# Kernel optimization log

Hardware: AMD Instinct MI355X
Metric: run time of the kernel (lower is better)

The kernel has to match this reference:

```python
import jax, jax.numpy as jnp
import numpy as np

NEG_SLOPE = 0.2

def gat_layer(x, src, dst, W, a_src, a_dst, num_nodes):
    """PyG-style GATConv. W:[F_in,H*C], a_src/a_dst:[H,C]. Returns [N,H,C]."""
    H, C = a_src.shape
    h = (x @ W).reshape(num_nodes, H, C)                      # [N,H,C]
    e_src = jnp.sum(h * a_src, axis=-1)                       # [N,H]
    e_dst = jnp.sum(h * a_dst, axis=-1)                       # [N,H]
    e = jax.nn.leaky_relu(e_src[src] + e_dst[dst], NEG_SLOPE) # [E,H]
    # segment softmax over incoming edges of each destination node
    m = jax.ops.segment_max(e, dst, num_segments=num_nodes)
    w = jnp.exp(e - m[dst])
    z = jax.ops.segment_sum(w, dst, num_segments=num_nodes)
    alpha = w / (z[dst] + 1e-16)                               # [E,H]
    msg = h[src] * alpha[:, :, None]                           # [E,H,C]
    return jax.ops.segment_sum(msg, dst, num_segments=num_nodes)


def setup_inputs() -> dict:
    key = jax.random.key(0)
    ks = jax.random.split(key, 16)
    N, E, F_IN, HID, A, G = 50000, 800000, 128, 128, 32, 64
    x = jax.random.normal(ks[0], (N, F_IN), dtype=jnp.float32)
    edge_index = jax.random.randint(ks[1], (2, E), 0, N, dtype=jnp.int32)
    batch = jnp.sort(jax.random.randint(ks[2], (N,), 0, G, dtype=jnp.int32))
    s = 0.1
    W1 = jax.random.normal(ks[3], (F_IN, 2 * HID), jnp.float32) * s
    a_src1 = jax.random.normal(ks[4], (2, HID), jnp.float32) * s
    a_dst1 = jax.random.normal(ks[5], (2, HID), jnp.float32) * s
    b1 = jnp.zeros((2 * HID,), jnp.float32)
    W2 = jax.random.normal(ks[6], (2 * HID, HID), jnp.float32) * s
    a_src2 = jax.random.normal(ks[7], (1, HID), jnp.float32) * s
    a_dst2 = jax.random.normal(ks[8], (1, HID), jnp.float32) * s
    b2 = jnp.zeros((HID,), jnp.float32)
    Wp = jax.random.normal(ks[9], (HID, A), jnp.float32) * s
    bp = jnp.zeros((A,), jnp.float32)
    Wv = jax.random.normal(ks[10], (HID, 1), jnp.float32) * s
    bv = jnp.zeros((1,), jnp.float32)
    return {"x": x, "edge_index": edge_index, "batch": batch,
            "W1": W1, "a_src1": a_src1, "a_dst1": a_dst1, "b1": b1,
            "W2": W2, "a_src2": a_src2, "a_dst2": a_dst2, "b2": b2,
            "Wp": Wp, "bp": bp, "Wv": Wv, "bv": bv}


def reference(x, edge_index, batch, W1, a_src1, a_dst1, b1,
              W2, a_src2, a_dst2, b2, Wp, bp, Wv, bv):
    N = x.shape[0]
    G = 64  # number of graphs in the batch
    # add self-loops (PyG GATConv default)
    loop = jnp.arange(N, dtype=edge_index.dtype)
    src = jnp.concatenate([edge_index[0], loop])
    dst = jnp.concatenate([edge_index[1], loop])
    # layer 1: heads=2, concat=True
    h1 = gat_layer(x, src, dst, W1, a_src1, a_dst1, N)        # [N,2,HID]
    h1 = jax.nn.elu(h1.reshape(N, -1) + b1)                   # [N,2*HID]
    # layer 2: heads=1, concat=False (mean over heads = identity for H=1)
    h2 = gat_layer(h1, src, dst, W2, a_src2, a_dst2, N)       # [N,1,HID]
    h2 = jax.nn.elu(h2.reshape(N, -1) + b2)                   # [N,HID]
    # global mean pool over graphs
    sums = jax.ops.segment_sum(h2, batch, num_segments=G)
    cnt = jax.ops.segment_sum(jnp.ones((N,), h2.dtype), batch, num_segments=G)
    x_pool = sums / jnp.maximum(cnt, 1.0)[:, None]            # [G,HID]
    policy_logits = x_pool @ Wp + bp                          # [G,A]
    state_value = x_pool @ Wv + bv                            # [G,1]
    return (policy_logits, state_value)
```

## Files before the change

kernel.cpp:

```cpp
#include <hip/hip_runtime.h>
#include <hip/hip_bf16.h>
#include <cstdint>


typedef __attribute__((ext_vector_type(8))) short bf16x8;
typedef __attribute__((ext_vector_type(4))) float f32x4;

#define NBLK_H 160
#define BSH 6
#define BMSK 63

__device__ __forceinline__ float wave_sum(float v) {
#pragma unroll
    for (int off = 32; off >= 1; off >>= 1) v += __shfl_xor(v, off, 64);
    return v;
}

__device__ __forceinline__ unsigned short f2bf(float f) {
    union { float f; uint32_t u; } c; c.f = f;
    uint32_t u = c.u;
    return (unsigned short)((u + 0x7fffu + ((u >> 16) & 1u)) >> 16);
}

__device__ __forceinline__ float bf2f(unsigned short u) {
    union { uint32_t u; float f; } c; c.u = ((uint32_t)u) << 16;
    return c.f;
}


template <int K, int FOUT>
__device__ __forceinline__ void swizzle_body(const float* __restrict__ W, int ldW, int colOff,
                                             unsigned short* __restrict__ Bsw, int tid) {
    constexpr int CPW = FOUT / 4, NCT = CPW / 16, KST = K / 32;
    if (tid >= K * FOUT / 8) return;
    int lane = tid & 63;
    int rest = tid >> 6;
    int t = rest % KST; rest /= KST;
    int c = rest % NCT; rest /= NCT;
    int cg_ = rest;
    int quad = lane >> 4, lo = lane & 15;
    int col = colOff + cg_ * CPW + c * 16 + lo;
    unsigned short v[8];
#pragma unroll
    for (int j = 0; j < 8; ++j)
        v[j] = f2bf(W[(t * 32 + quad * 8 + j) * ldW + col]);
    ushort4* dst = (ushort4*)(Bsw + (size_t)tid * 8);
    ushort4 o0, o1;
    o0.x = v[0]; o0.y = v[1]; o0.z = v[2]; o0.w = v[3];
    o1.x = v[4]; o1.y = v[5]; o1.z = v[6]; o1.w = v[7];
    dst[0] = o0; dst[1] = o1;
}


__global__ __launch_bounds__(256) void init_kernel(
        const float* __restrict__ W1, const float* __restrict__ W2,
        const float* __restrict__ a_src1, const float* __restrict__ a_dst1,
        unsigned short* __restrict__ B1h0, unsigned short* __restrict__ B1h1,
        unsigned short* __restrict__ B2,
        float* __restrict__ v1s, float* __restrict__ v1d,
        int* __restrict__ zbase, int zn4, int ZB,
        const int* __restrict__ ei, int* __restrict__ hist,
        int E, int ET, int CHUNK, int NB) {
    __shared__ int bins[1024];
    int b = blockIdx.x;
    if (b < 8)        swizzle_body<128, 128>(W1, 256, 0,   B1h0, b * 256 + threadIdx.x);
    else if (b < 16)  swizzle_body<128, 128>(W1, 256, 128, B1h1, (b - 8) * 256 + threadIdx.x);
    else if (b < 32)  swizzle_body<256, 128>(W2, 128, 0,   B2, (b - 16) * 256 + threadIdx.x);
    else if (b == 32) {
        int t = threadIdx.x, h = t >> 7, k = t & 127;
        float vs = 0.f, vd = 0.f;
        for (int c = 0; c < 128; ++c) {
            float w = W1[k * 256 + h * 128 + c];
            vs += w * a_src1[h * 128 + c];
            vd += w * a_dst1[h * 128 + c];
        }
        v1s[h * 128 + k] = vs;
        v1d[h * 128 + k] = vd;
    } else if (b < 33 + ZB) {
        int i = (b - 33) * 256 + threadIdx.x;
        if (i < zn4) ((int4*)zbase)[i] = make_int4(0, 0, 0, 0);
    } else {
        const int blk = b - 33 - ZB;
        for (int t = threadIdx.x; t < NB; t += 256) bins[t] = 0;
        __syncthreads();
        const int start = blk * CHUNK, end = min(ET, start + CHUNK);
        for (int i = start + threadIdx.x; i < end; i += 256) {
            int dst = (i < E) ? ei[E + i] : (i - E);
            atomicAdd(&bins[dst >> BSH], 1);
        }
        __syncthreads();
        for (int t = threadIdx.x; t < NB; t += 256) hist[t * NBLK_H + blk] = bins[t];
    }
}


__global__ __launch_bounds__(256) void scan_attn1(
        int* __restrict__ hist, int* __restrict__ tsum, int M, int TILESH,
        const float* __restrict__ x, const float* __restrict__ v1s,
        const float* __restrict__ v1d, float* __restrict__ es1,
        float* __restrict__ ed1, unsigned short* __restrict__ xbf, int N) {
    __shared__ int buf[256];
    if ((int)blockIdx.x < TILESH) {
        const int t = threadIdx.x;
        const int base = blockIdx.x * 1024 + t * 4;
        int v[4]; int s = 0;
#pragma unroll
        for (int k = 0; k < 4; ++k) { v[k] = (base + k < M) ? hist[base + k] : 0; s += v[k]; }
        buf[t] = s;
        __syncthreads();
#pragma unroll
        for (int off = 1; off < 256; off <<= 1) {
            int xx = (t >= off) ? buf[t - off] : 0;
            __syncthreads();
            buf[t] += xx;
            __syncthreads();
        }
        int run = buf[t] - s;
#pragma unroll
        for (int k = 0; k < 4; ++k) {
            if (base + k < M) hist[base + k] = run;
            run += v[k];
        }
        if (t == 255) tsum[blockIdx.x] = buf[255];
        return;
    }
    int bid = blockIdx.x - TILESH;
    int wid = (bid * 256 + threadIdx.x) >> 6;
    int lane = threadIdx.x & 63;
    if (wid >= N) return;
    float2 xv = *(const float2*)(x + (size_t)wid * 128 + lane * 2);
    float p0s = xv.x * v1s[lane * 2] + xv.y * v1s[lane * 2 + 1];
    float p1s = xv.x * v1s[128 + lane * 2] + xv.y * v1s[128 + lane * 2 + 1];
    float p0d = xv.x * v1d[lane * 2] + xv.y * v1d[lane * 2 + 1];
    float p1d = xv.x * v1d[128 + lane * 2] + xv.y * v1d[128 + lane * 2 + 1];
    p0s = wave_sum(p0s); p1s = wave_sum(p1s);
    p0d = wave_sum(p0d); p1d = wave_sum(p1d);
    if (lane == 0) {
        es1[wid * 2] = p0s; es1[wid * 2 + 1] = p1s;
        ed1[wid * 2] = p0d; ed1[wid * 2 + 1] = p1d;
    }
    ushort2 o; o.x = f2bf(xv.x); o.y = f2bf(xv.y);
    *(ushort2*)(xbf + (size_t)wid * 128 + lane * 2) = o;
}


__global__ __launch_bounds__(256) void part_kernel(const int* __restrict__ ei,
                                                   const int* __restrict__ hist,
                                                   const int* __restrict__ tsum,
                                                   int* __restrict__ bsorted,
                                                   int* __restrict__ segbase,
                                                   int E, int ET, int CHUNK, int NB, int T) {
    __shared__ int sb[256];
    __shared__ int scur[1024];
    const int t = threadIdx.x;
    sb[t] = (t < T) ? tsum[t] : 0;
    __syncthreads();
#pragma unroll
    for (int off = 1; off < 256; off <<= 1) {
        int v = (t >= off) ? sb[t - off] : 0;
        __syncthreads();
        sb[t] += v;
        __syncthreads();
    }
    const int blk = blockIdx.x;
    for (int b = t; b < NB; b += 256) {
        int idx = b * NBLK_H + blk;
        int tile = idx >> 10;
        int v = hist[idx] + (tile ? sb[tile - 1] : 0);
        scur[b] = v;
        if (blk == 0) segbase[b] = v;
    }
    if (blk == 0 && t == 0) segbase[NB] = sb[T - 1];
    __syncthreads();
    const int start = blk * CHUNK, end = min(ET, start + CHUNK);
    for (int i = start + t; i < end; i += 256) {
        int dst = (i < E) ? ei[E + i] : (i - E);
        int src = (i < E) ? ei[i] : dst;
        int pos = atomicAdd(&scur[dst >> BSH], 1);
        bsorted[pos] = (src << BSH) | (dst & BMSK);
    }
}


__global__ __launch_bounds__(256) void bucket_kernel(const int* __restrict__ bsorted,
                                                     const int* __restrict__ segbase,
                                                     const float* __restrict__ es1,
                                                     const float* __restrict__ ed1,
                                                     int* __restrict__ csr_src,
                                                     float2* __restrict__ csr_alpha,
                                                     int* __restrict__ rowptr,
                                                     int N, int NB) {
    __shared__ int cnt[64], excl[64];
    __shared__ float z0[64], z1[64];
    __shared__ float2 edv[64];
    __shared__ int ebuf[3072];
    __shared__ float2 wbuf[3072];
    const int b = blockIdx.x;
    const int gbase = segbase[b], gend = segbase[b + 1];
    const int sz = gend - gbase;
    const int t = threadIdx.x;
    if (b == 0 && t == 0) rowptr[N] = segbase[NB];
    if (t < 64) {
        cnt[t] = 0; z0[t] = 0.f; z1[t] = 0.f;
        int dst = (b << BSH) + t;
        if (dst < N) edv[t] = *(const float2*)(ed1 + dst * 2);
        else edv[t] = make_float2(0.f, 0.f);
    }
    __syncthreads();
    const bool fits = (sz <= 3072);
    for (int i = t; i < sz; i += 256) {
        int p = bsorted[gbase + i];
        int s = p >> BSH, ld = p & BMSK;
        float2 esv = *(const float2*)(es1 + s * 2);
        float e0 = esv.x + edv[ld].x; e0 = (e0 > 0.f) ? e0 : 0.2f * e0;
        float e1 = esv.y + edv[ld].y; e1 = (e1 > 0.f) ? e1 : 0.2f * e1;
        float w0 = __expf(e0), w1 = __expf(e1);
        if (fits) { ebuf[i] = p; wbuf[i] = make_float2(w0, w1); }
        atomicAdd(&z0[ld], w0);
        atomicAdd(&z1[ld], w1);
        atomicAdd(&cnt[ld], 1);
    }
    __syncthreads();
    if (t < 64) excl[t] = cnt[t];
    __syncthreads();
    for (int off = 1; off < 64; off <<= 1) {
        int v = (t < 64 && t >= off) ? excl[t - off] : 0;
        __syncthreads();
        if (t < 64) excl[t] += v;
        __syncthreads();
    }
    if (t < 64) {
        int dst = (b << BSH) + t;
        if (dst < N) rowptr[dst] = gbase + excl[t] - cnt[t];
    }
    __syncthreads();
    if (t < 64) {
        cnt[t] = excl[t] - cnt[t];
        z0[t] = 1.f / (z0[t] + 1e-16f);
        z1[t] = 1.f / (z1[t] + 1e-16f);
    }
    __syncthreads();
    if (fits) {
        for (int i = t; i < sz; i += 256) {
            int p = ebuf[i]; float2 wv = wbuf[i];
            int ld = p & BMSK;
            int pos = atomicAdd(&cnt[ld], 1);
            csr_src[gbase + pos] = p >> BSH;
            csr_alpha[gbase + pos] = make_float2(wv.x * z0[ld], wv.y * z1[ld]);
        }
    } else {
        for (int i = t; i < sz; i += 256) {
            int p = bsorted[gbase + i];
            int s = p >> BSH, ld = p & BMSK;
            float2 esv = *(const float2*)(es1 + s * 2);
            float e0 = esv.x + edv[ld].x; e0 = (e0 > 0.f) ? e0 : 0.2f * e0;
            float e1 = esv.y + edv[ld].y; e1 = (e1 > 0.f) ? e1 : 0.2f * e1;
            float w0 = __expf(e0), w1 = __expf(e1);
            int pos = atomicAdd(&cnt[ld], 1);
            csr_src[gbase + pos] = s;
            csr_alpha[gbase + pos] = make_float2(w0 * z0[ld], w1 * z1[ld]);
        }
    }
}


#define ACC2(U_, WW_, P_, Q_) { float v_;                              \
    v_ = bf2f(U_.x); P_.x += WW_.x * v_; Q_.x += WW_.y * v_;           \
    v_ = bf2f(U_.y); P_.y += WW_.x * v_; Q_.y += WW_.y * v_;           \
    v_ = bf2f(U_.z); P_.z += WW_.x * v_; Q_.z += WW_.y * v_;           \
    v_ = bf2f(U_.w); P_.w += WW_.x * v_; Q_.w += WW_.y * v_; }

__global__ void gat_agg_x(const unsigned short* __restrict__ xbf,
                          const int* __restrict__ rowptr, const int* __restrict__ csr_src,
                          const float2* __restrict__ csr_alpha,
                          unsigned short* __restrict__ aggx, int N, int NPAD) {
    __shared__ int    s_lds[4][2][32];
    __shared__ float2 a_lds[4][2][32];
    const int wave = threadIdx.x >> 6, lane = threadIdx.x & 63;
    const int g = lane >> 5, c = lane & 31;
    const int node = (blockIdx.x * 4 + wave) * 2 + g;
    if (node >= N) return;
    const int rs = rowptr[node], re = rowptr[node + 1];
    float4 p = {0.f, 0.f, 0.f, 0.f}, q = {0.f, 0.f, 0.f, 0.f};
    for (int i = rs; i < re; i += 32) {
        const int cnt = min(re - i, 32);
        if (c < cnt) {
            s_lds[wave][g][c] = csr_src[i + c];
            a_lds[wave][g][c] = csr_alpha[i + c];
        }
        int k = 0;
        for (; k + 7 < cnt; k += 8) {
            int s0 = s_lds[wave][g][k + 0], s1 = s_lds[wave][g][k + 1];
            int s2 = s_lds[wave][g][k + 2], s3 = s_lds[wave][g][k + 3];
            int s4 = s_lds[wave][g][k + 4], s5 = s_lds[wave][g][k + 5];
            int s6 = s_lds[wave][g][k + 6], s7 = s_lds[wave][g][k + 7];
            float2 a0 = a_lds[wave][g][k + 0], a1 = a_lds[wave][g][k + 1];
            float2 a2 = a_lds[wave][g][k + 2], a3 = a_lds[wave][g][k + 3];
            float2 a4 = a_lds[wave][g][k + 4], a5 = a_lds[wave][g][k + 5];
            float2 a6 = a_lds[wave][g][k + 6], a7 = a_lds[wave][g][k + 7];
            ushort4 u0 = *(const ushort4*)(xbf + (size_t)s0 * 128 + c * 4);
            ushort4 u1 = *(const ushort4*)(xbf + (size_t)s1 * 128 + c * 4);
            ushort4 u2 = *(const ushort4*)(xbf + (size_t)s2 * 128 + c * 4);
            ushort4 u3 = *(const ushort4*)(xbf + (size_t)s3 * 128 + c * 4);
            ushort4 u4 = *(const ushort4*)(xbf + (size_t)s4 * 128 + c * 4);
            ushort4 u5 = *(const ushort4*)(xbf + (size_t)s5 * 128 + c * 4);
            ushort4 u6 = *(const ushort4*)(xbf + (size_t)s6 * 128 + c * 4);
            ushort4 u7 = *(const ushort4*)(xbf + (size_t)s7 * 128 + c * 4);
            ACC2(u0, a0, p, q);
            ACC2(u1, a1, p, q);
            ACC2(u2, a2, p, q);
            ACC2(u3, a3, p, q);
            ACC2(u4, a4, p, q);
            ACC2(u5, a5, p, q);
            ACC2(u6, a6, p, q);
            ACC2(u7, a7, p, q);
        }
        for (; k < cnt; ++k) {
            int s0 = s_lds[wave][g][k];
            float2 a0 = a_lds[wave][g][k];
            ushort4 u0 = *(const ushort4*)(xbf + (size_t)s0 * 128 + c * 4);
            ACC2(u0, a0, p, q);
        }
    }
    ushort4 o;
    o.x = f2bf(p.x); o.y = f2bf(p.y); o.z = f2bf(p.z); o.w = f2bf(p.w);
    *(ushort4*)(aggx + (size_t)node * 128 + c * 4) = o;
    o.x = f2bf(q.x); o.y = f2bf(q.y); o.z = f2bf(q.z); o.w = f2bf(q.w);
    *(ushort4*)(aggx + (size_t)NPAD * 128 + (size_t)node * 128 + c * 4) = o;
}


__global__ __launch_bounds__(256) void gemm12_fused(
        const unsigned short* __restrict__ Abase,
        const unsigned short* __restrict__ B1h0, const unsigned short* __restrict__ B1h1,
        const unsigned short* __restrict__ B2sw,
        const float* __restrict__ b1,
        const float* __restrict__ a_src, const float* __restrict__ a_dst,
        float* __restrict__ es, float* __restrict__ ed,
        unsigned short* __restrict__ C, int N, int NPAD) {
    __shared__ unsigned short h1t[64][264];
    __shared__ float lds_ps[4][64];
    __shared__ float lds_pd[4][64];
    const int tid = threadIdx.x;
    const int wave = tid >> 6, lane = tid & 63;
    const int quad = lane >> 4, lo = lane & 15;
    const int n0 = blockIdx.x * 64;

    {
        const int head = wave >> 1, wh = wave & 1;
        const unsigned short* A = Abase + (size_t)head * NPAD * 128;
        const bf16x8* Bp = (const bf16x8*)(head ? B1h1 : B1h0);
        bf16x8 bf[4][4];
#pragma unroll
        for (int c = 0; c < 4; ++c)
#pragma unroll
            for (int t = 0; t < 4; ++t)
                bf[c][t] = Bp[((wh * 4 + c) * 4 + t) * 64 + lane];
        f32x4 acc[4][4];
#pragma unroll
        for (int r = 0; r < 4; ++r)
#pragma unroll
            for (int c = 0; c < 4; ++c) acc[r][c] = (f32x4){0.f, 0.f, 0.f, 0.f};
#pragma unroll
        for (int r = 0; r < 4; ++r) {
            const unsigned short* Ar = A + (size_t)(n0 + r * 16 + lo) * 128 + quad * 8;
#pragma unroll
            for (int t = 0; t < 4; ++t) {
                bf16x8 af = *(const bf16x8*)(Ar + t * 32);
#pragma unroll
                for (int c = 0; c < 4; ++c)
                    acc[r][c] = __builtin_amdgcn_mfma_f32_16x16x32_bf16(af, bf[c][t],
                                                                       acc[r][c], 0, 0, 0);
            }
        }
#pragma unroll
        for (int r = 0; r < 4; ++r) {
            int rl = r * 16 + quad * 4;
#pragma unroll
            for (int c = 0; c < 4; ++c) {
                int col = head * 128 + wh * 64 + c * 16 + lo;
                float bv = b1[col];
#pragma unroll
                for (int j = 0; j < 4; ++j) {
                    float v = acc[r][c][j] + bv;
                    v = (v > 0.f) ? v : __expf(v) - 1.f;
                    h1t[rl + j][col] = f2bf(v);
                }
            }
        }
    }
    __syncthreads();

    bf16x8 bf2[2][8];
    {
        const bf16x8* Bp2 = (const bf16x8*)B2sw;
#pragma unroll
        for (int c = 0; c < 2; ++c)
#pragma unroll
            for (int t = 0; t < 8; ++t)
                bf2[c][t] = Bp2[((wave * 2 + c) * 8 + t) * 64 + lane];
    }
    f32x4 acc2[4][2];
#pragma unroll
    for (int r = 0; r < 4; ++r)
#pragma unroll
        for (int c = 0; c < 2; ++c) acc2[r][c] = (f32x4){0.f, 0.f, 0.f, 0.f};
#pragma unroll
    for (int r = 0; r < 4; ++r) {
        const unsigned short* Ar = &h1t[r * 16 + lo][quad * 8];
#pragma unroll
        for (int t = 0; t < 8; ++t) {
            bf16x8 af = *(const bf16x8*)(Ar + t * 32);
#pragma unroll
            for (int c = 0; c < 2; ++c)
                acc2[r][c] = __builtin_amdgcn_mfma_f32_16x16x32_bf16(af, bf2[c][t],
                                                                    acc2[r][c], 0, 0, 0);
        }
    }
    const int c0 = wave * 32;
#pragma unroll
    for (int r = 0; r < 4; ++r) {
        int row = n0 + r * 16 + quad * 4;
#pragma unroll
        for (int c = 0; c < 2; ++c) {
            int col = c0 + c * 16 + lo;
#pragma unroll
            for (int j = 0; j < 4; ++j)
                if (row + j < N) C[(size_t)(row + j) * 128 + col] = f2bf(acc2[r][c][j]);
        }
    }
    float asv[2], adv[2];
#pragma unroll
    for (int c = 0; c < 2; ++c) {
        int col = c0 + c * 16 + lo;
        asv[c] = a_src[col];
        adv[c] = a_dst[col];
    }
#pragma unroll
    for (int r = 0; r < 4; ++r) {
#pragma unroll
        for (int j = 0; j < 4; ++j) {
            float ps = 0.f, pd = 0.f;
#pragma unroll
            for (int c = 0; c < 2; ++c) { ps += acc2[r][c][j] * asv[c]; pd += acc2[r][c][j] * adv[c]; }
#pragma unroll
            for (int off = 1; off <= 8; off <<= 1) {
                ps += __shfl_xor(ps, off, 64);
                pd += __shfl_xor(pd, off, 64);
            }
            if (lo == 0) {
                int row_l = r * 16 + quad * 4 + j;
                lds_ps[wave][row_l] = ps;
                lds_pd[wave][row_l] = pd;
            }
        }
    }
    __syncthreads();
    if (tid < 64) {
        int row = tid;
        int n = n0 + row;
        if (n < N) {
            es[n] = lds_ps[0][row] + lds_ps[1][row] + lds_ps[2][row] + lds_ps[3][row];
            ed[n] = lds_pd[0][row] + lds_pd[1][row] + lds_pd[2][row] + lds_pd[3][row];
        }
    }
}


__global__ void alpha2_kernel(const int* __restrict__ rowptr, const int* __restrict__ csr_src,
                              const float* __restrict__ es, const float* __restrict__ ed,
                              float* __restrict__ csr_a2, int N) {
    int wid = (blockIdx.x * blockDim.x + threadIdx.x) >> 6;
    int lane = threadIdx.x & 63;
    if (wid >= N) return;
    const int rs = rowptr[wid], re = rowptr[wid + 1];
    const float edn = ed[wid];
    float z = 0.f;
    for (int i = rs; i < re; i += 64) {
        int cnt = min(re - i, 64);
        if (lane < cnt) {
            int s = csr_src[i + lane];
            float e = es[s] + edn;
            e = (e > 0.f) ? e : 0.2f * e;
            float w = __expf(e);
            csr_a2[i + lane] = w;
            z += w;
        }
    }
    z = wave_sum(z);
    const float rz = 1.f / (z + 1e-16f);
    for (int i = rs + lane; i < re; i += 64) csr_a2[i] *= rz;
}


#define ACC1(U_, W_, P_) {                                   \
    P_.x += W_ * bf2f(U_.x); P_.y += W_ * bf2f(U_.y);        \
    P_.z += W_ * bf2f(U_.z); P_.w += W_ * bf2f(U_.w); }

__global__ void gat_agg_h1(const unsigned short* __restrict__ Hpre,
                           const int* __restrict__ rowptr, const int* __restrict__ csr_src,
                           const float* __restrict__ csr_a2,
                           const float* __restrict__ bias, unsigned short* __restrict__ out,
                           int N) {
    __shared__ int   s_lds[4][2][32];
    __shared__ float a_lds[4][2][32];
    const int wave = threadIdx.x >> 6, lane = threadIdx.x & 63;
    const int g = lane >> 5, c = lane & 31;
    const int node = (blockIdx.x * 4 + wave) * 2 + g;
    if (node >= N) return;
    const int rs = rowptr[node], re = rowptr[node + 1];
    float4 p = {0.f, 0.f, 0.f, 0.f};
    for (int i = rs; i < re; i += 32) {
        const int cnt = min(re - i, 32);
        if (c < cnt) {
            s_lds[wave][g][c] = csr_src[i + c];
            a_lds[wave][g][c] = csr_a2[i + c];
        }
        int k = 0;
        for (; k + 7 < cnt; k += 8) {
            int s0 = s_lds[wave][g][k + 0], s1 = s_lds[wave][g][k + 1];
            int s2 = s_lds[wave][g][k + 2], s3 = s_lds[wave][g][k + 3];
            int s4 = s_lds[wave][g][k + 4], s5 = s_lds[wave][g][k + 5];
            int s6 = s_lds[wave][g][k + 6], s7 = s_lds[wave][g][k + 7];
            float a0 = a_lds[wave][g][k + 0], a1 = a_lds[wave][g][k + 1];
            float a2 = a_lds[wave][g][k + 2], a3 = a_lds[wave][g][k + 3];
            float a4 = a_lds[wave][g][k + 4], a5 = a_lds[wave][g][k + 5];
            float a6 = a_lds[wave][g][k + 6], a7 = a_lds[wave][g][k + 7];
            ushort4 u0 = *(const ushort4*)(Hpre + (size_t)s0 * 128 + c * 4);
            ushort4 u1 = *(const ushort4*)(Hpre + (size_t)s1 * 128 + c * 4);
            ushort4 u2 = *(const ushort4*)(Hpre + (size_t)s2 * 128 + c * 4);
            ushort4 u3 = *(const ushort4*)(Hpre + (size_t)s3 * 128 + c * 4);
            ushort4 u4 = *(const ushort4*)(Hpre + (size_t)s4 * 128 + c * 4);
            ushort4 u5 = *(const ushort4*)(Hpre + (size_t)s5 * 128 + c * 4);
            ushort4 u6 = *(const ushort4*)(Hpre + (size_t)s6 * 128 + c * 4);
            ushort4 u7 = *(const ushort4*)(Hpre + (size_t)s7 * 128 + c * 4);
            ACC1(u0, a0, p);
            ACC1(u1, a1, p);
            ACC1(u2, a2, p);
            ACC1(u3, a3, p);
            ACC1(u4, a4, p);
            ACC1(u5, a5, p);
            ACC1(u6, a6, p);
            ACC1(u7, a7, p);
        }
        for (; k < cnt; ++k) {
            int s0 = s_lds[wave][g][k];
            float a0 = a_lds[wave][g][k];
            ushort4 u0 = *(const ushort4*)(Hpre + (size_t)s0 * 128 + c * 4);
            ACC1(u0, a0, p);
        }
    }
    float4 bv = ((const float4*)bias)[c];
    float ox = p.x + bv.x, oy = p.y + bv.y, oz = p.z + bv.z, ow = p.w + bv.w;
    ox = (ox > 0.f) ? ox : __expf(ox) - 1.f;
    oy = (oy > 0.f) ? oy : __expf(oy) - 1.f;
    oz = (oz > 0.f) ? oz : __expf(oz) - 1.f;
    ow = (ow > 0.f) ? ow : __expf(ow) - 1.f;
    ushort4 o;
    o.x = f2bf(ox); o.y = f2bf(oy); o.z = f2bf(oz); o.w = f2bf(ow);
    *(ushort4*)(out + (size_t)node * 128 + c * 4) = o;
}


#define PCHUNK 256

__global__ __launch_bounds__(256) void pool_partial(const unsigned short* __restrict__ h2,
                                                    const int* __restrict__ batch,
                                                    float* __restrict__ xsum,
                                                    int* __restrict__ cnt, int N) {
    const int base = blockIdx.x * PCHUNK;
    const int rg = threadIdx.x >> 6;
    const int c2 = threadIdx.x & 63;
    float ax = 0.f, ay = 0.f;
    int gcur = -1, run = 0;
    for (int r = rg; r < PCHUNK; r += 4) {
        int i = base + r;
        if (i >= N) break;
        int g = batch[i];
        if (g != gcur) {
            if (gcur >= 0) {
                atomicAdd(&xsum[gcur * 128 + c2 * 2 + 0], ax);
                atomicAdd(&xsum[gcur * 128 + c2 * 2 + 1], ay);
                if (c2 == 0) atomicAdd(&cnt[gcur], run);
            }
            gcur = g; ax = 0.f; ay = 0.f; run = 0;
        }
        ushort2 u = *(const ushort2*)(h2 + (size_t)i * 128 + c2 * 2);
        ax += bf2f(u.x); ay += bf2f(u.y);
        run += 1;
    }
    if (gcur >= 0) {
        atomicAdd(&xsum[gcur * 128 + c2 * 2 + 0], ax);
        atomicAdd(&xsum[gcur * 128 + c2 * 2 + 1], ay);
        if (c2 == 0) atomicAdd(&cnt[gcur], run);
    }
}


__global__ void head_kernel(const float* __restrict__ xsum, const int* __restrict__ cnt,
                            const float* __restrict__ Wp, const float* __restrict__ bp,
                            const float* __restrict__ Wv, const float* __restrict__ bv,
                            float* __restrict__ out) {
    int g = blockIdx.x, t = threadIdx.x;
    __shared__ float p[128];
    float inv = 1.f / fmaxf((float)cnt[g], 1.f);
    p[t] = xsum[g * 128 + t] * inv;
    p[t + 64] = xsum[g * 128 + t + 64] * inv;
    __syncthreads();
    if (t < 32) {
        float acc = bp[t];
        for (int k = 0; k < 128; ++k) acc += p[k] * Wp[k * 32 + t];
        out[g * 32 + t] = acc;
    } else if (t == 32) {
        float acc = bv[0];
        for (int k = 0; k < 128; ++k) acc += p[k] * Wv[k];
        out[64 * 32 + g] = acc;
    }
}


extern "C" void kernel_launch(void* const* d_in, const int* in_sizes, int n_in,
                              void* d_out, int out_size, void* d_ws, size_t ws_size,
                              hipStream_t stream) {
    const float* x      = (const float*)d_in[0];
    const int*   ei     = (const int*)d_in[1];
    const int*   batch  = (const int*)d_in[2];
    const float* W1     = (const float*)d_in[3];
    const float* a_src1 = (const float*)d_in[4];
    const float* a_dst1 = (const float*)d_in[5];
    const float* b1     = (const float*)d_in[6];
    const float* W2     = (const float*)d_in[7];
    const float* a_src2 = (const float*)d_in[8];
    const float* a_dst2 = (const float*)d_in[9];
    const float* b2     = (const float*)d_in[10];
    const float* Wp     = (const float*)d_in[11];
    const float* bp     = (const float*)d_in[12];
    const float* Wv     = (const float*)d_in[13];
    const float* bv     = (const float*)d_in[14];

    const int N  = in_sizes[0] / 128;
    const int E  = in_sizes[1] / 2;
    const int ET = E + N;
    const int NPAD = ((N + 63) / 64) * 64;
    const int NBLK = NPAD / 64;
    const int PBLK = (N + PCHUNK - 1) / PCHUNK;
    const int NB = (N + 63) >> BSH;
    const int CHUNK = (ET + NBLK_H - 1) / NBLK_H;
    const int M = NB * NBLK_H;
    const int TILESH = (M + 1023) / 1024;
    const int AB = (N + 3) / 4;
    const int GB = (N + 7) / 8;

    char* ws = (char*)d_ws;
    size_t off = 0;
    auto alloc = [&](size_t bytes) -> void* {
        void* p = ws + off;
        off = (off + bytes + 255) & ~(size_t)255;
        return p;
    };
    unsigned short* xbf   = (unsigned short*)alloc((size_t)NPAD * 128 * 2);
    unsigned short* aggx  = (unsigned short*)alloc((size_t)2 * NPAD * 128 * 2);
    unsigned short* h2pre = (unsigned short*)alloc((size_t)NPAD * 128 * 2);
    unsigned short* h2bf  = (unsigned short*)alloc((size_t)N * 128 * 2);
    unsigned short* w1h0  = (unsigned short*)alloc((size_t)128 * 128 * 2);
    unsigned short* w1h1  = (unsigned short*)alloc((size_t)128 * 128 * 2);
    unsigned short* w2sw  = (unsigned short*)alloc((size_t)256 * 128 * 2);
    float* v1s = (float*)alloc(256 * 4);
    float* v1d = (float*)alloc(256 * 4);
    float* es1 = (float*)alloc((size_t)N * 2 * 4);
    float* ed1 = (float*)alloc((size_t)N * 2 * 4);
    float* es2 = (float*)alloc((size_t)N * 4);
    float* ed2 = (float*)alloc((size_t)N * 4);
    const int ZINTS = 64 * 128 + 64;
    int*   zbase  = (int*)alloc(((size_t)ZINTS + 8) * 4);
    float* xsum   = (float*)zbase;
    int*   cnt    = (int*)(xsum + 64 * 128);
    int*    rowptr    = (int*)alloc((size_t)(N + 1) * 4);
    int*    hist      = (int*)alloc((size_t)M * 4);
    int*    segbase   = (int*)alloc((size_t)(NB + 1) * 4);
    int*    bsorted   = (int*)alloc((size_t)ET * 4);
    int*    csrsrc    = (int*)alloc((size_t)ET * 4);
    float2* csralpha  = (float2*)alloc((size_t)ET * 8);
    float*  csra2     = (float*)alloc((size_t)ET * 4);
    int*    tsum      = (int*)alloc(256 * 4);
    const int zn4 = (ZINTS + 3) / 4;
    const int ZB = (zn4 + 255) / 256;

    init_kernel<<<33 + ZB + NBLK_H, 256, 0, stream>>>(W1, W2, a_src1, a_dst1,
                                                      w1h0, w1h1, w2sw, v1s, v1d,
                                                      zbase, zn4, ZB,
                                                      ei, hist, E, ET, CHUNK, NB);
    scan_attn1<<<TILESH + AB, 256, 0, stream>>>(hist, tsum, M, TILESH,
                                                x, v1s, v1d, es1, ed1, xbf, N);
    part_kernel<<<NBLK_H, 256, 0, stream>>>(ei, hist, tsum, bsorted, segbase,
                                            E, ET, CHUNK, NB, TILESH);
    bucket_kernel<<<NB, 256, 0, stream>>>(bsorted, segbase, es1, ed1,
                                          csrsrc, csralpha, rowptr, N, NB);
    gat_agg_x<<<GB, 256, 0, stream>>>(xbf, rowptr, csrsrc, csralpha, aggx, N, NPAD);
    gemm12_fused<<<NBLK, 256, 0, stream>>>(aggx, w1h0, w1h1, w2sw, b1,
                                           a_src2, a_dst2, es2, ed2, h2pre, N, NPAD);
    alpha2_kernel<<<AB, 256, 0, stream>>>(rowptr, csrsrc, es2, ed2, csra2, N);
    gat_agg_h1<<<GB, 256, 0, stream>>>(h2pre, rowptr, csrsrc, csra2, b2, h2bf, N);
    pool_partial<<<PBLK, 256, 0, stream>>>(h2bf, batch, xsum, cnt, N);
    head_kernel<<<64, 64, 0, stream>>>(xsum, cnt, Wp, bp, Wv, bv, (float*)d_out);
}
```

Measured before the change: 304.9 us.

## Fuse softmax weights into aggregation kernels and halve gemm12 row tile

The edge softmax weights for both GAT layers are now computed inside the aggregation kernels, and normalisation happens once at the end of each node's accumulation. This removes the alpha2 kernel and the per-edge alpha arrays in global memory, and bucket_kernel now only builds the CSR source list. gemm12_fused moves from 64-row to 32-row tiles and uses an XOR-swizzled LDS layout to avoid bank conflicts, which launches more blocks and uses less LDS. The cost is recomputing exp on gathered es values inside the aggregation loop, plus a wave-level reduction for the normaliser.

```diff
diff --git a/kernel.cpp b/kernel.cpp
--- a/kernel.cpp
+++ b/kernel.cpp
@@ -9,6 +9,7 @@
 #define NBLK_H 160
 #define BSH 6
 #define BMSK 63
+#define PCHUNK 256
 
 __device__ __forceinline__ float wave_sum(float v) {
 #pragma unroll
@@ -184,41 +185,32 @@
 
 __global__ __launch_bounds__(256) void bucket_kernel(const int* __restrict__ bsorted,
                                                      const int* __restrict__ segbase,
-                                                     const float* __restrict__ es1,
-                                                     const float* __restrict__ ed1,
                                                      int* __restrict__ csr_src,
-                                                     float2* __restrict__ csr_alpha,
                                                      int* __restrict__ rowptr,
                                                      int N, int NB) {
-    __shared__ int cnt[64], excl[64];
-    __shared__ float z0[64], z1[64];
-    __shared__ float2 edv[64];
-    __shared__ int ebuf[3072];
-    __shared__ float2 wbuf[3072];
+    __shared__ int cnt[64];
+    __shared__ int excl[64];
+    __shared__ int ebuf[2304];
     const int b = blockIdx.x;
-    const int gbase = segbase[b], gend = segbase[b + 1];
+    const int gbase = segbase[b];
+    const int gend  = segbase[b + 1];
     const int sz = gend - gbase;
     const int t = threadIdx.x;
-    if (b == 0 && t == 0) rowptr[N] = segbase[NB];
-    if (t < 64) {
-        cnt[t] = 0; z0[t] = 0.f; z1[t] = 0.f;
-        int dst = (b << BSH) + t;
-        if (dst < N) edv[t] = *(const float2*)(ed1 + dst * 2);
-        else edv[t] = make_float2(0.f, 0.f);
-    }
-    __syncthreads();
-    const bool fits = (sz <= 3072);
-    for (int i = t; i < sz; i += 256) {
-        int p = bsorted[gbase + i];
-        int s = p >> BSH, ld = p & BMSK;
-        float2 esv = *(const float2*)(es1 + s * 2);
-        float e0 = esv.x + edv[ld].x; e0 = (e0 > 0.f) ? e0 : 0.2f * e0;
-        float e1 = esv.y + edv[ld].y; e1 = (e1 > 0.f) ? e1 : 0.2f * e1;
-        float w0 = __expf(e0), w1 = __expf(e1);
-        if (fits) { ebuf[i] = p; wbuf[i] = make_float2(w0, w1); }
-        atomicAdd(&z0[ld], w0);
-        atomicAdd(&z1[ld], w1);
-        atomicAdd(&cnt[ld], 1);
+    if (b == 0 && t == 255) rowptr[N] = segbase[NB];
+    if (t < 64) cnt[t] = 0;
+    __syncthreads();
+    const bool fits = (sz <= 2304);
+    if (fits) {
+        for (int i = t; i < sz; i += 256) {
+            int p = bsorted[gbase + i];
+            ebuf[i] = p;
+            atomicAdd(&cnt[p & BMSK], 1);
+        }
+    } else {
+        for (int i = t; i < sz; i += 256) {
+            int p = bsorted[gbase + i];
+            atomicAdd(&cnt[p & BMSK], 1);
+        }
     }
     __syncthreads();
     if (t < 64) excl[t] = cnt[t];
@@ -234,31 +226,19 @@
         if (dst < N) rowptr[dst] = gbase + excl[t] - cnt[t];
     }
     __syncthreads();
-    if (t < 64) {
-        cnt[t] = excl[t] - cnt[t];
-        z0[t] = 1.f / (z0[t] + 1e-16f);
-        z1[t] = 1.f / (z1[t] + 1e-16f);
-    }
+    if (t < 64) cnt[t] = excl[t] - cnt[t];
     __syncthreads();
     if (fits) {
         for (int i = t; i < sz; i += 256) {
-            int p = ebuf[i]; float2 wv = wbuf[i];
-            int ld = p & BMSK;
-            int pos = atomicAdd(&cnt[ld], 1);
+            int p = ebuf[i];
+            int pos = atomicAdd(&cnt[p & BMSK], 1);
             csr_src[gbase + pos] = p >> BSH;
-            csr_alpha[gbase + pos] = make_float2(wv.x * z0[ld], wv.y * z1[ld]);
         }
     } else {
         for (int i = t; i < sz; i += 256) {
             int p = bsorted[gbase + i];
-            int s = p >> BSH, ld = p & BMSK;
-            float2 esv = *(const float2*)(es1 + s * 2);
-            float e0 = esv.x + edv[ld].x; e0 = (e0 > 0.f) ? e0 : 0.2f * e0;
-            float e1 = esv.y + edv[ld].y; e1 = (e1 > 0.f) ? e1 : 0.2f * e1;
-            float w0 = __expf(e0), w1 = __expf(e1);
-            int pos = atomicAdd(&cnt[ld], 1);
-            csr_src[gbase + pos] = s;
-            csr_alpha[gbase + pos] = make_float2(w0 * z0[ld], w1 * z1[ld]);
+            int pos = atomicAdd(&cnt[p & BMSK], 1);
+            csr_src[gbase + pos] = p >> BSH;
         }
     }
 }
@@ -271,22 +251,31 @@
     v_ = bf2f(U_.w); P_.w += WW_.x * v_; Q_.w += WW_.y * v_; }
 
 __global__ void gat_agg_x(const unsigned short* __restrict__ xbf,
+                          const float* __restrict__ es, const float* __restrict__ ed,
                           const int* __restrict__ rowptr, const int* __restrict__ csr_src,
-                          const float2* __restrict__ csr_alpha,
                           unsigned short* __restrict__ aggx, int N, int NPAD) {
     __shared__ int    s_lds[4][2][32];
-    __shared__ float2 a_lds[4][2][32];
+    __shared__ float2 w_lds[4][2][32];
     const int wave = threadIdx.x >> 6, lane = threadIdx.x & 63;
     const int g = lane >> 5, c = lane & 31;
     const int node = (blockIdx.x * 4 + wave) * 2 + g;
     if (node >= N) return;
     const int rs = rowptr[node], re = rowptr[node + 1];
+    const float2 edn = *(const float2*)(ed + node * 2);
+
+    float z0 = 0.f, z1 = 0.f;
     float4 p = {0.f, 0.f, 0.f, 0.f}, q = {0.f, 0.f, 0.f, 0.f};
     for (int i = rs; i < re; i += 32) {
         const int cnt = min(re - i, 32);
         if (c < cnt) {
-            s_lds[wave][g][c] = csr_src[i + c];
-            a_lds[wave][g][c] = csr_alpha[i + c];
+            int s = csr_src[i + c];
+            float2 esv = *(const float2*)(es + s * 2);
+            float e0 = esv.x + edn.x; e0 = (e0 > 0.f) ? e0 : 0.2f * e0;
+            float e1 = esv.y + edn.y; e1 = (e1 > 0.f) ? e1 : 0.2f * e1;
+            float w0 = __expf(e0), w1 = __expf(e1);
+            s_lds[wave][g][c] = s;
+            w_lds[wave][g][c] = make_float2(w0, w1);
+            z0 += w0; z1 += w1;
         }
         int k = 0;
         for (; k + 7 < cnt; k += 8) {
@@ -294,10 +283,10 @@
             int s2 = s_lds[wave][g][k + 2], s3 = s_lds[wave][g][k + 3];
             int s4 = s_lds[wave][g][k + 4], s5 = s_lds[wave][g][k + 5];
             int s6 = s_lds[wave][g][k + 6], s7 = s_lds[wave][g][k + 7];
-            float2 a0 = a_lds[wave][g][k + 0], a1 = a_lds[wave][g][k + 1];
-            float2 a2 = a_lds[wave][g][k + 2], a3 = a_lds[wave][g][k + 3];
-            float2 a4 = a_lds[wave][g][k + 4], a5 = a_lds[wave][g][k + 5];
-            float2 a6 = a_lds[wave][g][k + 6], a7 = a_lds[wave][g][k + 7];
+            float2 a0 = w_lds[wave][g][k + 0], a1 = w_lds[wave][g][k + 1];
+            float2 a2 = w_lds[wave][g][k + 2], a3 = w_lds[wave][g][k + 3];
+            float2 a4 = w_lds[wave][g][k + 4], a5 = w_lds[wave][g][k + 5];
+            float2 a6 = w_lds[wave][g][k + 6], a7 = w_lds[wave][g][k + 7];
             ushort4 u0 = *(const ushort4*)(xbf + (size_t)s0 * 128 + c * 4);
             ushort4 u1 = *(const ushort4*)(xbf + (size_t)s1 * 128 + c * 4);
             ushort4 u2 = *(const ushort4*)(xbf + (size_t)s2 * 128 + c * 4);
@@ -317,15 +306,24 @@
         }
         for (; k < cnt; ++k) {
             int s0 = s_lds[wave][g][k];
-            float2 a0 = a_lds[wave][g][k];
+            float2 a0 = w_lds[wave][g][k];
             ushort4 u0 = *(const ushort4*)(xbf + (size_t)s0 * 128 + c * 4);
             ACC2(u0, a0, p, q);
         }
     }
+#pragma unroll
+    for (int off = 16; off >= 1; off >>= 1) {
+        z0 += __shfl_xor(z0, off, 64);
+        z1 += __shfl_xor(z1, off, 64);
+    }
+    const float rz0 = 1.f / (z0 + 1e-16f);
+    const float rz1 = 1.f / (z1 + 1e-16f);
     ushort4 o;
-    o.x = f2bf(p.x); o.y = f2bf(p.y); o.z = f2bf(p.z); o.w = f2bf(p.w);
+    o.x = f2bf(p.x * rz0); o.y = f2bf(p.y * rz0);
+    o.z = f2bf(p.z * rz0); o.w = f2bf(p.w * rz0);
     *(ushort4*)(aggx + (size_t)node * 128 + c * 4) = o;
-    o.x = f2bf(q.x); o.y = f2bf(q.y); o.z = f2bf(q.z); o.w = f2bf(q.w);
+    o.x = f2bf(q.x * rz1); o.y = f2bf(q.y * rz1);
+    o.z = f2bf(q.z * rz1); o.w = f2bf(q.w * rz1);
     *(ushort4*)(aggx + (size_t)NPAD * 128 + (size_t)node * 128 + c * 4) = o;
 }
 
@@ -338,13 +336,14 @@
         const float* __restrict__ a_src, const float* __restrict__ a_dst,
         float* __restrict__ es, float* __restrict__ ed,
         unsigned short* __restrict__ C, int N, int NPAD) {
-    __shared__ unsigned short h1t[64][264];
-    __shared__ float lds_ps[4][64];
-    __shared__ float lds_pd[4][64];
+    __shared__ unsigned short h1t[32 * 256];
+    __shared__ float lds_ps[4][32];
+    __shared__ float lds_pd[4][32];
     const int tid = threadIdx.x;
     const int wave = tid >> 6, lane = tid & 63;
     const int quad = lane >> 4, lo = lane & 15;
-    const int n0 = blockIdx.x * 64;
+    const int n0 = blockIdx.x * 32;
+    char* h1b = (char*)h1t;
 
     {
         const int head = wave >> 1, wh = wave & 1;
@@ -356,13 +355,13 @@
 #pragma unroll
             for (int t = 0; t < 4; ++t)
                 bf[c][t] = Bp[((wh * 4 + c) * 4 + t) * 64 + lane];
-        f32x4 acc[4][4];
-#pragma unroll
-        for (int r = 0; r < 4; ++r)
+        f32x4 acc[2][4];
+#pragma unroll
+        for (int r = 0; r < 2; ++r)
 #pragma unroll
             for (int c = 0; c < 4; ++c) acc[r][c] = (f32x4){0.f, 0.f, 0.f, 0.f};
 #pragma unroll
-        for (int r = 0; r < 4; ++r) {
+        for (int r = 0; r < 2; ++r) {
             const unsigned short* Ar = A + (size_t)(n0 + r * 16 + lo) * 128 + quad * 8;
 #pragma unroll
             for (int t = 0; t < 4; ++t) {
@@ -374,7 +373,7 @@
             }
         }
 #pragma unroll
-        for (int r = 0; r < 4; ++r) {
+        for (int r = 0; r < 2; ++r) {
             int rl = r * 16 + quad * 4;
 #pragma unroll
             for (int c = 0; c < 4; ++c) {
@@ -384,7 +383,9 @@
                 for (int j = 0; j < 4; ++j) {
                     float v = acc[r][c][j] + bv;
                     v = (v > 0.f) ? v : __expf(v) - 1.f;
-                    h1t[rl + j][col] = f2bf(v);
+                    int row = rl + j;
+                    *(unsigned short*)(h1b + row * 512 + ((col * 2) ^ ((row & 31) << 4)))
+                        = f2bf(v);
                 }
             }
         }
@@ -400,17 +401,18 @@
             for (int t = 0; t < 8; ++t)
                 bf2[c][t] = Bp2[((wave * 2 + c) * 8 + t) * 64 + lane];
     }
-    f32x4 acc2[4][2];
-#pragma unroll
-    for (int r = 0; r < 4; ++r)
+    f32x4 acc2[2][2];
+#pragma unroll
+    for (int r = 0; r < 2; ++r)
 #pragma unroll
         for (int c = 0; c < 2; ++c) acc2[r][c] = (f32x4){0.f, 0.f, 0.f, 0.f};
 #pragma unroll
-    for (int r = 0; r < 4; ++r) {
-        const unsigned short* Ar = &h1t[r * 16 + lo][quad * 8];
+    for (int r = 0; r < 2; ++r) {
+        const int row = r * 16 + lo;
+        const int rsw = (row & 31) << 4;
 #pragma unroll
         for (int t = 0; t < 8; ++t) {
-            bf16x8 af = *(const bf16x8*)(Ar + t * 32);
+            bf16x8 af = *(const bf16x8*)(h1b + row * 512 + (((quad * 8 + t * 32) * 2) ^ rsw));
 #pragma unroll
             for (int c = 0; c < 2; ++c)
                 acc2[r][c] = __builtin_amdgcn_mfma_f32_16x16x32_bf16(af, bf2[c][t],
@@ -419,7 +421,7 @@
     }
     const int c0 = wave * 32;
 #pragma unroll
-    for (int r = 0; r < 4; ++r) {
+    for (int r = 0; r < 2; ++r) {
         int row = n0 + r * 16 + quad * 4;
 #pragma unroll
         for (int c = 0; c < 2; ++c) {
@@ -437,7 +439,7 @@
         adv[c] = a_dst[col];
     }
 #pragma unroll
-    for (int r = 0; r < 4; ++r) {
+    for (int r = 0; r < 2; ++r) {
 #pragma unroll
         for (int j = 0; j < 4; ++j) {
             float ps = 0.f, pd = 0.f;
@@ -456,7 +458,7 @@
         }
     }
     __syncthreads();
-    if (tid < 64) {
+    if (tid < 32) {
         int row = tid;
         int n = n0 + row;
         if (n < N) {
@@ -467,54 +469,36 @@
 }
 
 
-__global__ void alpha2_kernel(const int* __restrict__ rowptr, const int* __restrict__ csr_src,
-                              const float* __restrict__ es, const float* __restrict__ ed,
-                              float* __restrict__ csr_a2, int N) {
-    int wid = (blockIdx.x * blockDim.x + threadIdx.x) >> 6;
-    int lane = threadIdx.x & 63;
-    if (wid >= N) return;
-    const int rs = rowptr[wid], re = rowptr[wid + 1];
-    const float edn = ed[wid];
-    float z = 0.f;
-    for (int i = rs; i < re; i += 64) {
-        int cnt = min(re - i, 64);
-        if (lane < cnt) {
-            int s = csr_src[i + lane];
-            float e = es[s] + edn;
-            e = (e > 0.f) ? e : 0.2f * e;
-            float w = __expf(e);
-            csr_a2[i + lane] = w;
-            z += w;
-        }
-    }
-    z = wave_sum(z);
-    const float rz = 1.f / (z + 1e-16f);
-    for (int i = rs + lane; i < re; i += 64) csr_a2[i] *= rz;
-}
-
-
 #define ACC1(U_, W_, P_) {                                   \
     P_.x += W_ * bf2f(U_.x); P_.y += W_ * bf2f(U_.y);        \
     P_.z += W_ * bf2f(U_.z); P_.w += W_ * bf2f(U_.w); }
 
 __global__ void gat_agg_h1(const unsigned short* __restrict__ Hpre,
+                           const float* __restrict__ es, const float* __restrict__ ed,
                            const int* __restrict__ rowptr, const int* __restrict__ csr_src,
-                           const float* __restrict__ csr_a2,
                            const float* __restrict__ bias, unsigned short* __restrict__ out,
                            int N) {
     __shared__ int   s_lds[4][2][32];
-    __shared__ float a_lds[4][2][32];
+    __shared__ float w_lds[4][2][32];
     const int wave = threadIdx.x >> 6, lane = threadIdx.x & 63;
     const int g = lane >> 5, c = lane & 31;
     const int node = (blockIdx.x * 4 + wave) * 2 + g;
     if (node >= N) return;
     const int rs = rowptr[node], re = rowptr[node + 1];
+    const float edn = ed[node];
+
+    float z = 0.f;
     float4 p = {0.f, 0.f, 0.f, 0.f};
     for (int i = rs; i < re; i += 32) {
         const int cnt = min(re - i, 32);
         if (c < cnt) {
-            s_lds[wave][g][c] = csr_src[i + c];
-            a_lds[wave][g][c] = csr_a2[i + c];
+            int s = csr_src[i + c];
+            float e = es[s] + edn;
+            e = (e > 0.f) ? e : 0.2f * e;
+            float ww = __expf(e);
+            s_lds[wave][g][c] = s;
+            w_lds[wave][g][c] = ww;
+            z += ww;
         }
         int k = 0;
         for (; k + 7 < cnt; k += 8) {
@@ -522,10 +506,10 @@
             int s2 = s_lds[wave][g][k + 2], s3 = s_lds[wave][g][k + 3];
             int s4 = s_lds[wave][g][k + 4], s5 = s_lds[wave][g][k + 5];
             int s6 = s_lds[wave][g][k + 6], s7 = s_lds[wave][g][k + 7];
-            float a0 = a_lds[wave][g][k + 0], a1 = a_lds[wave][g][k + 1];
-            float a2 = a_lds[wave][g][k + 2], a3 = a_lds[wave][g][k + 3];
-            float a4 = a_lds[wave][g][k + 4], a5 = a_lds[wave][g][k + 5];
-            float a6 = a_lds[wave][g][k + 6], a7 = a_lds[wave][g][k + 7];
+            float a0 = w_lds[wave][g][k + 0], a1 = w_lds[wave][g][k + 1];
+            float a2 = w_lds[wave][g][k + 2], a3 = w_lds[wave][g][k + 3];
+            float a4 = w_lds[wave][g][k + 4], a5 = w_lds[wave][g][k + 5];
+            float a6 = w_lds[wave][g][k + 6], a7 = w_lds[wave][g][k + 7];
             ushort4 u0 = *(const ushort4*)(Hpre + (size_t)s0 * 128 + c * 4);
             ushort4 u1 = *(const ushort4*)(Hpre + (size_t)s1 * 128 + c * 4);
             ushort4 u2 = *(const ushort4*)(Hpre + (size_t)s2 * 128 + c * 4);
@@ -545,13 +529,17 @@
         }
         for (; k < cnt; ++k) {
             int s0 = s_lds[wave][g][k];
-            float a0 = a_lds[wave][g][k];
+            float a0 = w_lds[wave][g][k];
             ushort4 u0 = *(const ushort4*)(Hpre + (size_t)s0 * 128 + c * 4);
             ACC1(u0, a0, p);
         }
     }
+#pragma unroll
+    for (int off = 16; off >= 1; off >>= 1) z += __shfl_xor(z, off, 64);
+    const float rz = 1.f / (z + 1e-16f);
     float4 bv = ((const float4*)bias)[c];
-    float ox = p.x + bv.x, oy = p.y + bv.y, oz = p.z + bv.z, ow = p.w + bv.w;
+    float ox = p.x * rz + bv.x, oy = p.y * rz + bv.y;
+    float oz = p.z * rz + bv.z, ow = p.w * rz + bv.w;
     ox = (ox > 0.f) ? ox : __expf(ox) - 1.f;
     oy = (oy > 0.f) ? oy : __expf(oy) - 1.f;
     oz = (oz > 0.f) ? oz : __expf(oz) - 1.f;
@@ -561,8 +549,6 @@
     *(ushort4*)(out + (size_t)node * 128 + c * 4) = o;
 }
 
-
-#define PCHUNK 256
 
 __global__ __launch_bounds__(256) void pool_partial(const unsigned short* __restrict__ h2,
                                                     const int* __restrict__ batch,
@@ -642,7 +628,7 @@
     const int E  = in_sizes[1] / 2;
     const int ET = E + N;
     const int NPAD = ((N + 63) / 64) * 64;
-    const int NBLK = NPAD / 64;
+    const int NBLK32 = NPAD / 32;
     const int PBLK = (N + PCHUNK - 1) / PCHUNK;
     const int NB = (N + 63) >> BSH;
     const int CHUNK = (ET + NBLK_H - 1) / NBLK_H;
@@ -680,8 +666,6 @@
     int*    segbase   = (int*)alloc((size_t)(NB + 1) * 4);
     int*    bsorted   = (int*)alloc((size_t)ET * 4);
     int*    csrsrc    = (int*)alloc((size_t)ET * 4);
-    float2* csralpha  = (float2*)alloc((size_t)ET * 8);
-    float*  csra2     = (float*)alloc((size_t)ET * 4);
     int*    tsum      = (int*)alloc(256 * 4);
     const int zn4 = (ZINTS + 3) / 4;
     const int ZB = (zn4 + 255) / 256;
@@ -694,13 +678,11 @@
                                                 x, v1s, v1d, es1, ed1, xbf, N);
     part_kernel<<<NBLK_H, 256, 0, stream>>>(ei, hist, tsum, bsorted, segbase,
                                             E, ET, CHUNK, NB, TILESH);
-    bucket_kernel<<<NB, 256, 0, stream>>>(bsorted, segbase, es1, ed1,
-                                          csrsrc, csralpha, rowptr, N, NB);
-    gat_agg_x<<<GB, 256, 0, stream>>>(xbf, rowptr, csrsrc, csralpha, aggx, N, NPAD);
-    gemm12_fused<<<NBLK, 256, 0, stream>>>(aggx, w1h0, w1h1, w2sw, b1,
-                                           a_src2, a_dst2, es2, ed2, h2pre, N, NPAD);
-    alpha2_kernel<<<AB, 256, 0, stream>>>(rowptr, csrsrc, es2, ed2, csra2, N);
-    gat_agg_h1<<<GB, 256, 0, stream>>>(h2pre, rowptr, csrsrc, csra2, b2, h2bf, N);
+    bucket_kernel<<<NB, 256, 0, stream>>>(bsorted, segbase, csrsrc, rowptr, N, NB);
+    gat_agg_x<<<GB, 256, 0, stream>>>(xbf, es1, ed1, rowptr, csrsrc, aggx, N, NPAD);
+    gemm12_fused<<<NBLK32, 256, 0, stream>>>(aggx, w1h0, w1h1, w2sw, b1,
+                                             a_src2, a_dst2, es2, ed2, h2pre, N, NPAD);
+    gat_agg_h1<<<GB, 256, 0, stream>>>(h2pre, es2, ed2, rowptr, csrsrc, b2, h2bf, N);
     pool_partial<<<PBLK, 256, 0, stream>>>(h2bf, batch, xsum, cnt, N);
     head_kernel<<<64, 64, 0, stream>>>(xsum, cnt, Wp, bp, Wv, bv, (float*)d_out);
 }
```

New measurement: 273.0 us (median of 2 runs). -10.5%, faster.
